# Optimization experiments

Measured on AMD Instinct MI355X. Metric: run time of the kernel, lower is better.

## Reference

```python
import jax, jax.numpy as jnp
import numpy as np

T = 5          # Newton-Schulz iterations
EPS = 1e-5
NC = 64        # num_channels per group

def setup_inputs() -> dict:
    key = jax.random.key(0)
    X = jax.random.normal(key, (128, 256, 32, 32), dtype=jnp.float32)
    weight = jnp.ones((1, 256, 1, 1), dtype=jnp.float32)
    bias = jnp.zeros((1, 256, 1, 1), dtype=jnp.float32)
    return {"X": X, "weight": weight, "bias": bias}

def _iternorm(X):
    B, C, H, W = X.shape
    g = C // NC
    # [B,C,H,W] -> [C,B,H,W] -> [g, nc, m]
    x = jnp.transpose(X, (1, 0, 2, 3)).reshape(g, NC, -1)
    m = x.shape[-1]
    mean = x.mean(-1, keepdims=True)
    xc = x - mean                                   # [g, nc, m]
    I = jnp.eye(NC, dtype=X.dtype)
    Sigma = EPS * I + jnp.einsum('gdm,gem->gde', xc, xc) / m
    # rTr = 1 / trace(Sigma) per group
    rTr = 1.0 / jnp.trace(Sigma, axis1=1, axis2=2)[:, None, None]
    Sn = Sigma * rTr                                # normalized covariance
    P = jnp.broadcast_to(I, (g, NC, NC))
    for _ in range(T):
        P3 = jnp.matmul(jnp.matmul(P, P), P)
        P = 1.5 * P - 0.5 * jnp.matmul(P3, Sn)
    wm = P * jnp.sqrt(rTr)                          # whitening matrix [g,nc,nc]
    xn = jnp.matmul(wm, xc)                         # [g, nc, m]
    Xn = jnp.transpose(xn.reshape(C, B, H, W), (1, 0, 2, 3))
    return Xn

def reference(X, weight, bias):
    Xn = _iternorm(X)
    return Xn * weight + bias
```

## Files before the change

kernel.cpp:

```cpp
#include <hip/hip_runtime.h>
#include <hip/hip_bf16.h>
#include <cstddef>
#include <cstdint>

typedef __attribute__((ext_vector_type(8))) short s16x8;
typedef __attribute__((ext_vector_type(4))) short s16x4;
typedef __attribute__((ext_vector_type(4))) float f32x4;

namespace {
constexpr int NB   = 128;
constexpr int NCH  = 256;
constexpr int SPA  = 1024;
constexpr int NCC  = 64;
constexpr int MT   = NB * SPA;
constexpr float EPSV = 1e-5f;
}

__device__ inline unsigned short f2bf(float f) {
    union { float f; unsigned u; } v; v.f = f;
    unsigned r = v.u + 0x7fffu + ((v.u >> 16) & 1u);
    return (unsigned short)(r >> 16);
}

__device__ inline s16x8 cvt8(float4 a, float4 b) {
    union { __hip_bfloat162 h[4]; s16x8 s; } u;
    u.h[0] = __float22bfloat162_rn(make_float2(a.x, a.y));
    u.h[1] = __float22bfloat162_rn(make_float2(a.z, a.w));
    u.h[2] = __float22bfloat162_rn(make_float2(b.x, b.y));
    u.h[3] = __float22bfloat162_rn(make_float2(b.z, b.w));
    return u.s;
}

__device__ inline s16x8 pack8(const float* v) {
    union { __hip_bfloat162 h[4]; s16x8 s; } u;
    u.h[0] = __float22bfloat162_rn(make_float2(v[0], v[1]));
    u.h[1] = __float22bfloat162_rn(make_float2(v[2], v[3]));
    u.h[2] = __float22bfloat162_rn(make_float2(v[4], v[5]));
    u.h[3] = __float22bfloat162_rn(make_float2(v[6], v[7]));
    return u.s;
}

__device__ inline void issue8(const float* const base[4], int ks, float4 r[4][2]) {
#pragma unroll
    for (int cb = 0; cb < 4; ++cb) {
        r[cb][0] = *reinterpret_cast<const float4*>(base[cb] + ks * 32);
        r[cb][1] = *reinterpret_cast<const float4*>(base[cb] + ks * 32 + 4);
    }
}
__device__ inline void finish8(const float4 r[4][2], s16x8 frag[4], float csum[4]) {
#pragma unroll
    for (int cb = 0; cb < 4; ++cb) {
        const float4 f0 = r[cb][0], f1 = r[cb][1];
        csum[cb] += (f0.x + f0.y) + (f0.z + f0.w) + (f1.x + f1.y) + (f1.z + f1.w);
        frag[cb] = cvt8(f0, f1);
    }
}
__device__ inline void mfma10(const s16x8 frag[4], f32x4 acc[10]) {
    int n = 0;
#pragma unroll
    for (int i = 0; i < 4; ++i)
#pragma unroll
        for (int j = i; j < 4; ++j) {
            acc[n] = __builtin_amdgcn_mfma_f32_16x16x32_bf16(frag[i], frag[j], acc[n], 0, 0, 0);
            ++n;
        }
}

__global__ __launch_bounds__(256) void zca_stats(const float* __restrict__ X,
                                                 float* __restrict__ Gpart,
                                                 float* __restrict__ Spart) {
    const int bid = blockIdx.x;
    const int g = bid >> 7, b = bid & 127;
    const int t = threadIdx.x;
    const int w = t >> 6, l = t & 63;
    const int lr = l & 15, gq = l >> 4;

    const float* xs = X + ((size_t)b * NCH + (size_t)g * NCC) * SPA;

    const float* base[4];
#pragma unroll
    for (int cb = 0; cb < 4; ++cb)
        base[cb] = xs + (size_t)(cb * 16 + lr) * SPA + w * 256 + gq * 8;

    f32x4 acc[10];
#pragma unroll
    for (int n = 0; n < 10; ++n) acc[n] = (f32x4){0.f, 0.f, 0.f, 0.f};
    float csum[4] = {0.f, 0.f, 0.f, 0.f};

    float4 rA[4][2], rB[4][2];
    issue8(base, 0, rA);
    issue8(base, 1, rB);
#pragma unroll
    for (int ks = 0; ks < 8; ks += 2) {
        s16x8 frag[4];
        finish8(rA, frag, csum);
        if (ks + 2 < 8) issue8(base, ks + 2, rA);
        mfma10(frag, acc);
        finish8(rB, frag, csum);
        if (ks + 3 < 8) issue8(base, ks + 3, rB);
        mfma10(frag, acc);
    }

    __shared__ float Gl[64 * 67];
    __shared__ float Ssl[4][64];

#pragma unroll
    for (int cb = 0; cb < 4; ++cb) {
        float s = csum[cb];
        s += __shfl_xor(s, 16, 64);
        s += __shfl_xor(s, 32, 64);
        if (gq == 0) Ssl[w][cb * 16 + lr] = s;
    }

    for (int ph = 0; ph < 4; ++ph) {
        if (w == ph) {
            int n = 0;
#pragma unroll
            for (int i = 0; i < 4; ++i)
#pragma unroll
                for (int j = i; j < 4; ++j) {
#pragma unroll
                    for (int q = 0; q < 4; ++q) {
                        const int d = i * 16 + gq * 4 + q;
                        const int e = j * 16 + lr;
                        const float val = acc[n][q];
                        if (ph == 0) {
                            Gl[d * 67 + e] = val;
                            if (i != j) Gl[e * 67 + d] = val;
                        } else {
                            Gl[d * 67 + e] += val;
                            if (i != j) Gl[e * 67 + d] += val;
                        }
                    }
                    ++n;
                }
        }
        __syncthreads();
    }

#pragma unroll
    for (int i = 0; i < 16; ++i) {
        const int idx = i * 256 + t;
        const int d = idx >> 6, e = idx & 63;
        Gpart[(size_t)bid * 4096 + idx] = Gl[d * 67 + e];
    }
    if (t < 64)
        Spart[(size_t)bid * 64 + t] =
            ((Ssl[0][t] + Ssl[1][t]) + (Ssl[2][t] + Ssl[3][t]));
}

__global__ __launch_bounds__(256) void zca_reduce(const float* __restrict__ Gpart,
                                                  const float* __restrict__ Spart,
                                                  float* __restrict__ Gsum,
                                                  float* __restrict__ Ssub) {
    const int g = blockIdx.x >> 4, eb = blockIdx.x & 15;
    const int t = threadIdx.x;
    const float* p = Gpart + (size_t)g * 128 * 4096 + eb * 256 + t;
    float a0 = 0.f, a1 = 0.f, a2 = 0.f, a3 = 0.f;
    for (int q = 0; q < 128; q += 4) {
        a0 += p[(size_t)(q + 0) * 4096];
        a1 += p[(size_t)(q + 1) * 4096];
        a2 += p[(size_t)(q + 2) * 4096];
        a3 += p[(size_t)(q + 3) * 4096];
    }
    Gsum[(size_t)g * 4096 + eb * 256 + t] = (a0 + a1) + (a2 + a3);

    if (t < 64) {
        float s = 0.f;
        for (int q = 0; q < 8; ++q)
            s += Spart[(size_t)(g * 128 + eb * 8 + q) * 64 + t];
        Ssub[(size_t)(g * 16 + eb) * 64 + t] = s;
    }
}

__global__ __launch_bounds__(256) void zca_newton(const float* __restrict__ Gsum,
                                                  const float* __restrict__ Ssub,
                                                  const float* __restrict__ weight,
                                                  const float* __restrict__ bias,
                                                  short* __restrict__ wmB,
                                                  float* __restrict__ betaOut) {
    const int g = blockIdx.x;
    const int t = threadIdx.x;
    const int v = t >> 4;
    const int u = t & 15;
    const int e0 = 4 * u;

    __shared__ float Pm[64 * 68];
    __shared__ float Sn[64 * 68];
    __shared__ float Ta[64 * 68];
    __shared__ float meanS[64];
    __shared__ float scal[2];

    if (t < 64) {
        float s = 0.f;
        for (int eb = 0; eb < 16; ++eb) s += Ssub[(size_t)(g * 16 + eb) * 64 + t];
        meanS[t] = s * (1.0f / MT);
    }
    __syncthreads();

#pragma unroll
    for (int i = 0; i < 4; ++i) {
        const int d = v + 16 * i;
        float4 gv = *reinterpret_cast<const float4*>(Gsum + (size_t)g * 4096 + d * 64 + e0);
        const float md = meanS[d];
        float vals[4] = {gv.x, gv.y, gv.z, gv.w};
#pragma unroll
        for (int c = 0; c < 4; ++c)
            Sn[d * 68 + e0 + c] = vals[c] * (1.0f / MT) - md * meanS[e0 + c]
                                  + ((d == e0 + c) ? EPSV : 0.f);
    }
    __syncthreads();

    if (t < 64) {
        float tr = Sn[t * 68 + t];
        for (int off = 32; off > 0; off >>= 1) tr += __shfl_down(tr, off, 64);
        if (t == 0) {
            scal[0] = 1.0f / tr;
            scal[1] = sqrtf(1.0f / tr);
        }
    }
    __syncthreads();
    const float rTr = scal[0];

#pragma unroll
    for (int i = 0; i < 4; ++i) {
        const int d = v + 16 * i;
#pragma unroll
        for (int c = 0; c < 4; ++c) {
            Sn[d * 68 + e0 + c] *= rTr;
            Pm[d * 68 + e0 + c] = (d == e0 + c) ? 1.f : 0.f;
        }
    }
    __syncthreads();

    auto mm = [&](const float* A, const float* Bm, float r[4][4]) {
#pragma unroll
        for (int i = 0; i < 4; ++i)
#pragma unroll
            for (int c = 0; c < 4; ++c) r[i][c] = 0.f;
        for (int k = 0; k < 64; ++k) {
            float a[4];
#pragma unroll
            for (int i = 0; i < 4; ++i) a[i] = A[(v + 16 * i) * 68 + k];
            const float4 bv = *reinterpret_cast<const float4*>(Bm + k * 68 + e0);
#pragma unroll
            for (int i = 0; i < 4; ++i) {
                r[i][0] += a[i] * bv.x;
                r[i][1] += a[i] * bv.y;
                r[i][2] += a[i] * bv.z;
                r[i][3] += a[i] * bv.w;
            }
        }
    };
    auto storeTa = [&](const float r[4][4]) {
#pragma unroll
        for (int i = 0; i < 4; ++i) {
            float4 o = {r[i][0], r[i][1], r[i][2], r[i][3]};
            *reinterpret_cast<float4*>(&Ta[(v + 16 * i) * 68 + e0]) = o;
        }
    };

    for (int it = 0; it < 5; ++it) {
        float r[4][4];
        mm(Pm, Sn, r);
        storeTa(r);
        __syncthreads();
        mm(Pm, Ta, r);
        __syncthreads();
        storeTa(r);
        __syncthreads();
        mm(Pm, Ta, r);
        __syncthreads();
#pragma unroll
        for (int i = 0; i < 4; ++i) {
            const int d = v + 16 * i;
#pragma unroll
            for (int c = 0; c < 4; ++c)
                Pm[d * 68 + e0 + c] = 1.5f * Pm[d * 68 + e0 + c] - 0.5f * r[i][c];
        }
        __syncthreads();
    }

    const float srTr = scal[1];
#pragma unroll
    for (int i = 0; i < 4; ++i) {
        const int d = v + 16 * i;
        const float wv = weight[g * NCC + d];
        s16x4 pk;
#pragma unroll
        for (int c = 0; c < 4; ++c)
            pk[c] = (short)f2bf(Pm[d * 68 + e0 + c] * srTr * wv);
        *reinterpret_cast<s16x4*>(wmB + (size_t)g * 4096 + d * 64 + e0) = pk;
    }
    if (t < 64) {
        int d = t;
        float s = 0.f;
        for (int e = 0; e < 64; ++e) s += Pm[d * 68 + e] * meanS[e];
        betaOut[g * NCC + d] = bias[g * NCC + d] - weight[g * NCC + d] * srTr * s;
    }
}

__global__ __launch_bounds__(256) void zca_apply(const float* __restrict__ X,
                                                 const short* __restrict__ wmB,
                                                 const float* __restrict__ beta,
                                                 float* __restrict__ out) {
    const int bid = blockIdx.x;
    const int g  = bid & 3;
    const int qm = (bid >> 2) & 3;
    const int b  = bid >> 4;
    const int t  = threadIdx.x;
    const int w  = t >> 6, l = t & 63;
    const int lr = l & 15, gq = l >> 4;

    __shared__ float Xt[2][64][64];
    __shared__ float Ot[64][68];

    s16x8 wa[4][2];
#pragma unroll
    for (int i = 0; i < 4; ++i)
#pragma unroll
        for (int kc = 0; kc < 2; ++kc)
            wa[i][kc] = *reinterpret_cast<const s16x8*>(
                wmB + (size_t)g * 4096 + (16 * i + lr) * 64 + kc * 32 + gq * 8);

    const int ch = t >> 4, s4 = t & 15;
    float bst[4];
#pragma unroll
    for (int i = 0; i < 4; ++i) bst[i] = beta[g * NCC + i * 16 + ch];

    const float* xb = X + ((size_t)b * NCH + (size_t)g * NCC) * SPA + qm * 256;
    float* ob = out + ((size_t)b * NCH + (size_t)g * NCC) * SPA + qm * 256;

    const int lh = l >> 4;

    auto stage = [&](int tile, int buf) {
#pragma unroll
        for (int i = 0; i < 4; ++i) {
            const float* gsrc = xb + (size_t)(i * 16 + w * 4 + lh) * SPA
                                + tile * 64 + (l & 15) * 4;
            __builtin_amdgcn_global_load_lds(
                (const __attribute__((address_space(1))) void*)gsrc,
                (__attribute__((address_space(3))) void*)&Xt[buf][i * 16 + w * 4][0],
                16, 0, 0);
        }
    };

    stage(0, 0);
    asm volatile("s_waitcnt vmcnt(0)" ::: "memory");
    __syncthreads();

    for (int tile = 0; tile < 4; ++tile) {
        const int buf = tile & 1;
        if (tile + 1 < 4) stage(tile + 1, buf ^ 1);

        float v[2][8];
#pragma unroll
        for (int kc = 0; kc < 2; ++kc)
#pragma unroll
            for (int j = 0; j < 8; ++j)
                v[kc][j] = Xt[buf][kc * 32 + gq * 8 + j][w * 16 + lr];

        s16x8 bf0 = pack8(v[0]);
        s16x8 bf1 = pack8(v[1]);

        f32x4 acc[4];
#pragma unroll
        for (int i = 0; i < 4; ++i) acc[i] = (f32x4){0.f, 0.f, 0.f, 0.f};
#pragma unroll
        for (int i = 0; i < 4; ++i) {
            acc[i] = __builtin_amdgcn_mfma_f32_16x16x32_bf16(wa[i][0], bf0, acc[i], 0, 0, 0);
            acc[i] = __builtin_amdgcn_mfma_f32_16x16x32_bf16(wa[i][1], bf1, acc[i], 0, 0, 0);
        }

        __syncthreads();

#pragma unroll
        for (int i = 0; i < 4; ++i)
#pragma unroll
            for (int q = 0; q < 4; ++q)
                Ot[16 * i + 4 * gq + q][w * 16 + lr] = acc[i][q];

        asm volatile("s_waitcnt vmcnt(0)" ::: "memory");
        __syncthreads();

#pragma unroll
        for (int i = 0; i < 4; ++i) {
            float4 o = *reinterpret_cast<const float4*>(&Ot[i * 16 + ch][s4 * 4]);
            o.x += bst[i]; o.y += bst[i]; o.z += bst[i]; o.w += bst[i];
            *reinterpret_cast<float4*>(
                ob + (size_t)(i * 16 + ch) * SPA + tile * 64 + s4 * 4) = o;
        }
    }
}

extern "C" void kernel_launch(void* const* d_in, const int* in_sizes, int n_in,
                              void* d_out, int out_size, void* d_ws, size_t ws_size,
                              hipStream_t stream) {
    const float* X      = (const float*)d_in[0];
    const float* weight = (const float*)d_in[1];
    const float* bias   = (const float*)d_in[2];
    float* out = (float*)d_out;

    float* ws    = (float*)d_ws;
    float* Gpart = ws;
    float* Spart = Gpart + (size_t)512 * 4096;
    float* Gsum  = Spart + (size_t)512 * 64;
    float* Ssub  = Gsum + (size_t)4 * 4096;
    float* betaW = Ssub + (size_t)4 * 16 * 64;
    short* wmB   = (short*)(betaW + 256);

    zca_stats <<<dim3(512),  dim3(256), 0, stream>>>(X, Gpart, Spart);
    zca_reduce<<<dim3(64),   dim3(256), 0, stream>>>(Gpart, Spart, Gsum, Ssub);
    zca_newton<<<dim3(4),    dim3(256), 0, stream>>>(Gsum, Ssub, weight, bias, wmB, betaW);
    zca_apply <<<dim3(2048), dim3(256), 0, stream>>>(X, wmB, betaW, out);
}
```

Measured before the change: 121.8 us.

## Stage stats-kernel input via double-buffered global_load_lds and split MFMA work across waves

The covariance/stats kernel stops loading X directly into registers. It now streams 64-column tiles into a double-buffered LDS area with async global-to-LDS loads, overlapping the next tile's fetch with the current tile's compute. Wave pairs split the 10 symmetric MFMA blocks five and five, which halves the accumulator registers per wave, and one wave of each pair computes the channel sums. The cost is a barrier and a full vmcnt wait every tile, plus LDS reads that were not there before.

```diff
diff --git a/kernel.cpp b/kernel.cpp
--- a/kernel.cpp
+++ b/kernel.cpp
@@ -38,32 +38,6 @@
     u.h[2] = __float22bfloat162_rn(make_float2(v[4], v[5]));
     u.h[3] = __float22bfloat162_rn(make_float2(v[6], v[7]));
     return u.s;
-}
-
-__device__ inline void issue8(const float* const base[4], int ks, float4 r[4][2]) {
-#pragma unroll
-    for (int cb = 0; cb < 4; ++cb) {
-        r[cb][0] = *reinterpret_cast<const float4*>(base[cb] + ks * 32);
-        r[cb][1] = *reinterpret_cast<const float4*>(base[cb] + ks * 32 + 4);
-    }
-}
-__device__ inline void finish8(const float4 r[4][2], s16x8 frag[4], float csum[4]) {
-#pragma unroll
-    for (int cb = 0; cb < 4; ++cb) {
-        const float4 f0 = r[cb][0], f1 = r[cb][1];
-        csum[cb] += (f0.x + f0.y) + (f0.z + f0.w) + (f1.x + f1.y) + (f1.z + f1.w);
-        frag[cb] = cvt8(f0, f1);
-    }
-}
-__device__ inline void mfma10(const s16x8 frag[4], f32x4 acc[10]) {
-    int n = 0;
-#pragma unroll
-    for (int i = 0; i < 4; ++i)
-#pragma unroll
-        for (int j = i; j < 4; ++j) {
-            acc[n] = __builtin_amdgcn_mfma_f32_16x16x32_bf16(frag[i], frag[j], acc[n], 0, 0, 0);
-            ++n;
-        }
 }
 
 __global__ __launch_bounds__(256) void zca_stats(const float* __restrict__ X,
@@ -74,69 +48,108 @@
     const int t = threadIdx.x;
     const int w = t >> 6, l = t & 63;
     const int lr = l & 15, gq = l >> 4;
-
-    const float* xs = X + ((size_t)b * NCH + (size_t)g * NCC) * SPA;
-
-    const float* base[4];
-#pragma unroll
-    for (int cb = 0; cb < 4; ++cb)
-        base[cb] = xs + (size_t)(cb * 16 + lr) * SPA + w * 256 + gq * 8;
-
-    f32x4 acc[10];
-#pragma unroll
-    for (int n = 0; n < 10; ++n) acc[n] = (f32x4){0.f, 0.f, 0.f, 0.f};
+    const int h    = w >> 1;
+    const int half = w & 1;
+
+    __shared__ float smem[2 * 64 * 64];
+    float (*Xt)[64][64] = (float (*)[64][64])smem;
+
+    const float* xb = X + ((size_t)b * NCH + (size_t)g * NCC) * SPA;
+    const int lh = l >> 4;
+
+    auto stage = [&](int tile, int buf) {
+#pragma unroll
+        for (int i = 0; i < 4; ++i) {
+            const float* gsrc = xb + (size_t)(i * 16 + w * 4 + lh) * SPA
+                                + tile * 64 + (l & 15) * 4;
+            __builtin_amdgcn_global_load_lds(
+                (const __attribute__((address_space(1))) void*)gsrc,
+                (__attribute__((address_space(3))) void*)&Xt[buf][i * 16 + w * 4][0],
+                16, 0, 0);
+        }
+    };
+
+    f32x4 acc[5];
+#pragma unroll
+    for (int n = 0; n < 5; ++n) acc[n] = (f32x4){0.f, 0.f, 0.f, 0.f};
     float csum[4] = {0.f, 0.f, 0.f, 0.f};
 
-    float4 rA[4][2], rB[4][2];
-    issue8(base, 0, rA);
-    issue8(base, 1, rB);
-#pragma unroll
-    for (int ks = 0; ks < 8; ks += 2) {
+    stage(0, 0);
+    asm volatile("s_waitcnt vmcnt(0)" ::: "memory");
+    __syncthreads();
+
+    for (int tile = 0; tile < 16; ++tile) {
+        const int buf = tile & 1;
+        if (tile + 1 < 16) stage(tile + 1, buf ^ 1);
+
         s16x8 frag[4];
-        finish8(rA, frag, csum);
-        if (ks + 2 < 8) issue8(base, ks + 2, rA);
-        mfma10(frag, acc);
-        finish8(rB, frag, csum);
-        if (ks + 3 < 8) issue8(base, ks + 3, rB);
-        mfma10(frag, acc);
-    }
-
-    __shared__ float Gl[64 * 67];
-    __shared__ float Ssl[4][64];
-
-#pragma unroll
-    for (int cb = 0; cb < 4; ++cb) {
-        float s = csum[cb];
-        s += __shfl_xor(s, 16, 64);
-        s += __shfl_xor(s, 32, 64);
-        if (gq == 0) Ssl[w][cb * 16 + lr] = s;
-    }
-
-    for (int ph = 0; ph < 4; ++ph) {
-        if (w == ph) {
-            int n = 0;
-#pragma unroll
-            for (int i = 0; i < 4; ++i)
-#pragma unroll
-                for (int j = i; j < 4; ++j) {
-#pragma unroll
-                    for (int q = 0; q < 4; ++q) {
-                        const int d = i * 16 + gq * 4 + q;
-                        const int e = j * 16 + lr;
-                        const float val = acc[n][q];
-                        if (ph == 0) {
-                            Gl[d * 67 + e] = val;
-                            if (i != j) Gl[e * 67 + d] = val;
-                        } else {
-                            Gl[d * 67 + e] += val;
-                            if (i != j) Gl[e * 67 + d] += val;
-                        }
-                    }
-                    ++n;
-                }
-        }
-        __syncthreads();
-    }
+#pragma unroll
+        for (int cb = 0; cb < 4; ++cb) {
+            const float* row = &Xt[buf][cb * 16 + lr][h * 32 + gq * 8];
+            float4 f0 = *reinterpret_cast<const float4*>(row);
+            float4 f1 = *reinterpret_cast<const float4*>(row + 4);
+            if (half == 0)
+                csum[cb] += (f0.x + f0.y) + (f0.z + f0.w) + (f1.x + f1.y) + (f1.z + f1.w);
+            frag[cb] = cvt8(f0, f1);
+        }
+
+        if (half == 0) {
+            acc[0] = __builtin_amdgcn_mfma_f32_16x16x32_bf16(frag[0], frag[0], acc[0], 0, 0, 0);
+            acc[1] = __builtin_amdgcn_mfma_f32_16x16x32_bf16(frag[0], frag[1], acc[1], 0, 0, 0);
+            acc[2] = __builtin_amdgcn_mfma_f32_16x16x32_bf16(frag[0], frag[2], acc[2], 0, 0, 0);
+            acc[3] = __builtin_amdgcn_mfma_f32_16x16x32_bf16(frag[0], frag[3], acc[3], 0, 0, 0);
+            acc[4] = __builtin_amdgcn_mfma_f32_16x16x32_bf16(frag[1], frag[1], acc[4], 0, 0, 0);
+        } else {
+            acc[0] = __builtin_amdgcn_mfma_f32_16x16x32_bf16(frag[1], frag[2], acc[0], 0, 0, 0);
+            acc[1] = __builtin_amdgcn_mfma_f32_16x16x32_bf16(frag[1], frag[3], acc[1], 0, 0, 0);
+            acc[2] = __builtin_amdgcn_mfma_f32_16x16x32_bf16(frag[2], frag[2], acc[2], 0, 0, 0);
+            acc[3] = __builtin_amdgcn_mfma_f32_16x16x32_bf16(frag[2], frag[3], acc[3], 0, 0, 0);
+            acc[4] = __builtin_amdgcn_mfma_f32_16x16x32_bf16(frag[3], frag[3], acc[4], 0, 0, 0);
+        }
+
+        asm volatile("s_waitcnt vmcnt(0)" ::: "memory");
+        __syncthreads();
+    }
+
+    float* Gl  = smem;
+    float* Ssl = smem + 4288;
+
+    if (half == 0) {
+#pragma unroll
+        for (int cb = 0; cb < 4; ++cb) {
+            float s = csum[cb];
+            s += __shfl_xor(s, 16, 64);
+            s += __shfl_xor(s, 32, 64);
+            if (gq == 0) Ssl[w * 64 + cb * 16 + lr] = s;
+        }
+    }
+
+    auto emit = [&](int i, int j, int slot, bool first) {
+#pragma unroll
+        for (int q = 0; q < 4; ++q) {
+            const int d = i * 16 + gq * 4 + q;
+            const int e = j * 16 + lr;
+            const float val = acc[slot][q];
+            if (first) {
+                Gl[d * 67 + e] = val;
+                if (i != j) Gl[e * 67 + d] = val;
+            } else {
+                Gl[d * 67 + e] += val;
+                if (i != j) Gl[e * 67 + d] += val;
+            }
+        }
+    };
+
+    if (h == 0) {
+        if (half == 0) { emit(0,0,0,true); emit(0,1,1,true); emit(0,2,2,true); emit(0,3,3,true); emit(1,1,4,true); }
+        else           { emit(1,2,0,true); emit(1,3,1,true); emit(2,2,2,true); emit(2,3,3,true); emit(3,3,4,true); }
+    }
+    __syncthreads();
+    if (h == 1) {
+        if (half == 0) { emit(0,0,0,false); emit(0,1,1,false); emit(0,2,2,false); emit(0,3,3,false); emit(1,1,4,false); }
+        else           { emit(1,2,0,false); emit(1,3,1,false); emit(2,2,2,false); emit(2,3,3,false); emit(3,3,4,false); }
+    }
+    __syncthreads();
 
 #pragma unroll
     for (int i = 0; i < 16; ++i) {
@@ -145,8 +158,7 @@
         Gpart[(size_t)bid * 4096 + idx] = Gl[d * 67 + e];
     }
     if (t < 64)
-        Spart[(size_t)bid * 64 + t] =
-            ((Ssl[0][t] + Ssl[1][t]) + (Ssl[2][t] + Ssl[3][t]));
+        Spart[(size_t)bid * 64 + t] = Ssl[0 * 64 + t] + Ssl[2 * 64 + t];
 }
 
 __global__ __launch_bounds__(256) void zca_reduce(const float* __restrict__ Gpart,
```

New measurement: 117.0 us. 1.04x faster.
